# Kernel tuning notes

Measured on AMD Instinct MI355X. Metric: run time of the kernel, lower is better.

## Reference

```python
import jax, jax.numpy as jnp
import numpy as np
import math

B, P, C, PS = 128, 196, 3, 16      # batch, num_patchs, channels, patch_size
HID, HEADS, HD, FF = 768, 12, 64, 3072
RATE = PS // 4                      # highpass_rate = 4 -> rate = 4
EPS = 1e-5


def _local_highpass(x):
    # x: (B, P, HID) -> per-patch FFT highpass, matching LocalHighPass+HighPass.
    img = x.reshape(B, P, C, PS, PS)
    f = jnp.fft.fftshift(jnp.fft.fft2(img, norm='ortho'), axes=(-2, -1))
    mid = PS // 2
    f = f.at[..., mid - RATE:mid + RATE, mid - RATE:mid + RATE].set(0.0)
    out = jnp.fft.ifft2(jnp.fft.ifftshift(f, axes=(-2, -1)), norm='ortho').real
    return out.reshape(B, P, HID)


def _layernorm(x, g, b):
    m = x.mean(-1, keepdims=True)
    v = ((x - m) ** 2).mean(-1, keepdims=True)
    return (x - m) * jax.lax.rsqrt(v + EPS) * g + b


def setup_inputs() -> dict:
    key = jax.random.key(0)
    ks = jax.random.split(key, 16)
    s_h = 1.0 / math.sqrt(HID)
    s_f = 1.0 / math.sqrt(FF)
    inp = {
        'x': jax.random.normal(ks[0], (B, P, HID), jnp.float32),
        'q_w': jax.random.uniform(ks[1], (HID, HID), jnp.float32, -s_h, s_h),
        'q_b': jnp.zeros((HID,), jnp.float32),
        'k_w': jax.random.uniform(ks[2], (HID, HID), jnp.float32, -s_h, s_h),
        'k_b': jnp.zeros((HID,), jnp.float32),
        'v_w': jax.random.uniform(ks[3], (HID, HID), jnp.float32, -s_h, s_h),
        'v_b': jnp.zeros((HID,), jnp.float32),
        'w1': jax.random.uniform(ks[4], (FF, HID), jnp.float32, -s_h, s_h),
        'b1': jnp.zeros((FF,), jnp.float32),
        'w2': jax.random.uniform(ks[5], (HID, FF), jnp.float32, -s_f, s_f),
        'b2': jnp.zeros((HID,), jnp.float32),
        'ln0_g': jnp.ones((HID,), jnp.float32), 'ln0_b': jnp.zeros((HID,), jnp.float32),
        'ln1_g': jnp.ones((HID,), jnp.float32), 'ln1_b': jnp.zeros((HID,), jnp.float32),
        'ln2_g': jnp.ones((HID,), jnp.float32), 'ln2_b': jnp.zeros((HID,), jnp.float32),
    }
    return inp


def reference(x, q_w, q_b, k_w, k_b, v_w, v_b, w1, b1, w2, b2,
              ln0_g, ln0_b, ln1_g, ln1_b, ln2_g, ln2_b):
    hp = _local_highpass(x)                              # (B, P, HID)
    h = _layernorm(hp, ln0_g, ln0_b)
    # MSAttention (first_block=False, so no position embedding add)
    q = (h @ q_w.T + q_b).reshape(B, P, HEADS, HD)
    k = (h @ k_w.T + k_b).reshape(B, P, HEADS, HD)
    v = (h @ v_w.T + v_b).reshape(B, P, HEADS, HD)
    scores = jnp.einsum('bqhd,bkhd->bhqk', q, k) / math.sqrt(HD)
    probs = jax.nn.softmax(scores, axis=-1)
    ctx = jnp.einsum('bhqk,bkhd->bqhd', probs, v).reshape(B, P, HID)
    h2 = hp + _layernorm(ctx, ln1_g, ln1_b)
    mlp = jax.nn.relu(h2 @ w1.T + b1) @ w2.T + b2
    return h2 + _layernorm(mlp, ln2_g, ln2_b)
```

## Files before the change

kernel.cpp:

```cpp
#include <hip/hip_runtime.h>

#define NTOK   25088
#define HIDD   768
#define NHEAD  12
#define HDIM   64
#define FFD    3072
#define NPAT   196
#define QKVS   2304

typedef __attribute__((ext_vector_type(8))) short short8;
typedef __attribute__((ext_vector_type(8))) __bf16 bf16x8;
typedef __attribute__((ext_vector_type(4))) float f32x4;
typedef __attribute__((ext_vector_type(4))) float fl4;
typedef __attribute__((ext_vector_type(4))) unsigned short us4;
typedef __attribute__((ext_vector_type(8))) unsigned short us8;

#define AS1 __attribute__((address_space(1)))
#define AS3 __attribute__((address_space(3)))

__device__ __forceinline__ unsigned short f2bf(float f) {
  unsigned int u = __builtin_bit_cast(unsigned int, f);
  u += 0x7FFFu + ((u >> 16) & 1u);
  return (unsigned short)(u >> 16);
}
__device__ __forceinline__ float bf2f(unsigned short h) {
  unsigned int u = ((unsigned int)h) << 16;
  return __builtin_bit_cast(float, u);
}

template <typename A>
__device__ __forceinline__ auto mfma_sel(A a, A b, f32x4 c, int)
    -> decltype(__builtin_amdgcn_mfma_f32_16x16x32_bf16(a, b, c, 0, 0, 0)) {
  return __builtin_amdgcn_mfma_f32_16x16x32_bf16(a, b, c, 0, 0, 0);
}
template <typename A>
__device__ __forceinline__ auto mfma_sel(A a, A b, f32x4 c, long)
    -> decltype(__builtin_amdgcn_mfma_f32_16x16x32_bf16(
           __builtin_bit_cast(bf16x8, a), __builtin_bit_cast(bf16x8, b), c, 0, 0, 0)) {
  return __builtin_amdgcn_mfma_f32_16x16x32_bf16(
      __builtin_bit_cast(bf16x8, a), __builtin_bit_cast(bf16x8, b), c, 0, 0, 0);
}
__device__ __forceinline__ f32x4 MFMA16(short8 a, short8 b, f32x4 c) {
  return mfma_sel(a, b, c, 0);
}

__device__ __forceinline__ void gload16(const void* g, void* l) {
  __builtin_amdgcn_global_load_lds((const AS1 void*)g, (AS3 void*)l, 16, 0, 0);
}

__device__ __forceinline__ int swz_bid(int nwg) {
  int orig = (int)blockIdx.x;
  int xcd = orig & 7;
  int q = nwg >> 3, r = nwg & 7;
  int base = (xcd < r) ? xcd * (q + 1) : r * (q + 1) + (xcd - r) * q;
  return base + (orig >> 3);
}

__global__ __launch_bounds__(256) void build_M(unsigned short* __restrict__ Mb) {
  __shared__ float Cs[16], Ss[16];
  int t = threadIdx.x;
  if (t < 16) {
    float c = 0.f;
    for (int k = -4; k <= 3; ++k) c += cosf(0.39269908169872414f * (float)(k * t));
    Cs[t] = c;
    Ss[t] = -sinf(1.5707963267948966f * (float)t);
  }
  __syncthreads();
  int r = t >> 4, cc = t & 15;
  for (int j = 0; j < 256; ++j) {
    int dr = (r - (j >> 4)) & 15;
    int dc = (cc - (j & 15)) & 15;
    float val = ((t == j) ? 1.f : 0.f) - (Cs[dr] * Cs[dc] - Ss[dr] * Ss[dc]) * 0.00390625f;
    Mb[t * 256 + j] = f2bf(val);
  }
}

__global__ __launch_bounds__(256) void castk(const float* __restrict__ s,
                                             unsigned short* __restrict__ d, long n4) {
  for (long i = (long)blockIdx.x * 256 + threadIdx.x; i < n4; i += (long)gridDim.x * 256) {
    fl4 v = *(const fl4*)(s + i * 4);
    us4 o;
    o[0] = f2bf(v[0]); o[1] = f2bf(v[1]); o[2] = f2bf(v[2]); o[3] = f2bf(v[3]);
    *(us4*)(d + i * 4) = o;
  }
}

__global__ __launch_bounds__(256) void bias_cat(const float* __restrict__ qb,
                                                const float* __restrict__ kb,
                                                const float* __restrict__ vb,
                                                float* __restrict__ d) {
  for (int i = threadIdx.x; i < QKVS; i += 256)
    d[i] = (i < 768) ? qb[i] : (i < 1536) ? kb[i - 768] : vb[i - 1536];
}

template <int OUT_BF16, int BIAS, int RELU>
__global__ __launch_bounds__(256) void gemm_bt(const unsigned short* __restrict__ A,
                                               const unsigned short* __restrict__ Bm,
                                               const float* __restrict__ bias,
                                               void* __restrict__ Cp,
                                               int Mdim, int Ndim, int Kdim) {
  __shared__ __align__(16) unsigned short As[128 * 32];
  __shared__ __align__(16) unsigned short Bs[128 * 32];
  const int nbn = Ndim >> 7;
  const int bid = swz_bid((int)gridDim.x);
  const int bm = bid / nbn, bn = bid % nbn;
  const int t = threadIdx.x;
  const int lane = t & 63;
  const int w = t >> 6;
  const int wr = (w >> 1) * 64, wc = (w & 1) * 64;
  const int lm = lane & 15, lk = (lane >> 4) * 8;

  f32x4 acc[4][4];
#pragma unroll
  for (int i = 0; i < 4; ++i)
#pragma unroll
    for (int j = 0; j < 4; ++j) acc[i][j] = (f32x4){0.f, 0.f, 0.f, 0.f};

  const unsigned short* Ab = A + (size_t)(bm * 128 + (t >> 2)) * Kdim + (t & 3) * 8;
  const unsigned short* Bb = Bm + (size_t)(bn * 128 + (t >> 2)) * Kdim + (t & 3) * 8;
  unsigned short* AsP = As + t * 8;
  unsigned short* BsP = Bs + t * 8;

  for (int k0 = 0; k0 < Kdim; k0 += 32) {
    gload16(Ab + k0, AsP);
    gload16(Ab + (size_t)64 * Kdim + k0, AsP + 2048);
    gload16(Bb + k0, BsP);
    gload16(Bb + (size_t)64 * Kdim + k0, BsP + 2048);
    asm volatile("s_waitcnt vmcnt(0)" ::: "memory");
    __syncthreads();
    short8 af[4], bfr[4];
#pragma unroll
    for (int mi = 0; mi < 4; ++mi) af[mi] = *(const short8*)&As[(wr + mi * 16 + lm) * 32 + lk];
#pragma unroll
    for (int ni = 0; ni < 4; ++ni) bfr[ni] = *(const short8*)&Bs[(wc + ni * 16 + lm) * 32 + lk];
#pragma unroll
    for (int mi = 0; mi < 4; ++mi)
#pragma unroll
      for (int ni = 0; ni < 4; ++ni) acc[mi][ni] = MFMA16(af[mi], bfr[ni], acc[mi][ni]);
    __syncthreads();
  }

  const int row0 = bm * 128 + wr + (lane >> 4) * 4;
  const int col0 = bn * 128 + wc + lm;
#pragma unroll
  for (int mi = 0; mi < 4; ++mi) {
#pragma unroll
    for (int ni = 0; ni < 4; ++ni) {
      int col = col0 + ni * 16;
      float bia = BIAS ? bias[col] : 0.f;
#pragma unroll
      for (int rg = 0; rg < 4; ++rg) {
        int row = row0 + mi * 16 + rg;
        float vv = acc[mi][ni][rg] + bia;
        if (RELU) vv = vv > 0.f ? vv : 0.f;
        if (OUT_BF16)
          ((unsigned short*)Cp)[(size_t)row * Ndim + col] = f2bf(vv);
        else
          ((float*)Cp)[(size_t)row * Ndim + col] = vv;
      }
    }
  }
}

__global__ __launch_bounds__(256) void ln0_k(const unsigned short* __restrict__ x,
                                             const float* __restrict__ g,
                                             const float* __restrict__ bb,
                                             unsigned short* __restrict__ out) {
  int w = threadIdx.x >> 6, lane = threadIdx.x & 63;
  long row = (long)blockIdx.x * 4 + w;
  const unsigned short* xr = x + row * HIDD;
  float xv[12];
  float s1 = 0.f, s2 = 0.f;
#pragma unroll
  for (int c = 0; c < 3; ++c) {
    us4 u = *(const us4*)(xr + c * 256 + lane * 4);
#pragma unroll
    for (int j = 0; j < 4; ++j) {
      float f = bf2f(u[j]);
      xv[c * 4 + j] = f; s1 += f; s2 += f * f;
    }
  }
#pragma unroll
  for (int off = 32; off; off >>= 1) { s1 += __shfl_xor(s1, off); s2 += __shfl_xor(s2, off); }
  float m = s1 * (1.f / 768.f);
  float rs = rsqrtf(s2 * (1.f / 768.f) - m * m + 1e-5f);
#pragma unroll
  for (int c = 0; c < 3; ++c) {
    int cb = c * 256 + lane * 4;
    us4 o;
#pragma unroll
    for (int j = 0; j < 4; ++j) o[j] = f2bf((xv[c * 4 + j] - m) * rs * g[cb + j] + bb[cb + j]);
    *(us4*)(out + row * HIDD + cb) = o;
  }
}

__global__ __launch_bounds__(256) void ln1_k(const unsigned short* __restrict__ ctx,
                                             const unsigned short* __restrict__ hp,
                                             const float* __restrict__ g,
                                             const float* __restrict__ bb,
                                             float* __restrict__ h2f,
                                             unsigned short* __restrict__ h2b) {
  int w = threadIdx.x >> 6, lane = threadIdx.x & 63;
  long row = (long)blockIdx.x * 4 + w;
  const unsigned short* xr = ctx + row * HIDD;
  float xv[12];
  float s1 = 0.f, s2 = 0.f;
#pragma unroll
  for (int c = 0; c < 3; ++c) {
    us4 u = *(const us4*)(xr + c * 256 + lane * 4);
#pragma unroll
    for (int j = 0; j < 4; ++j) {
      float f = bf2f(u[j]);
      xv[c * 4 + j] = f; s1 += f; s2 += f * f;
    }
  }
#pragma unroll
  for (int off = 32; off; off >>= 1) { s1 += __shfl_xor(s1, off); s2 += __shfl_xor(s2, off); }
  float m = s1 * (1.f / 768.f);
  float rs = rsqrtf(s2 * (1.f / 768.f) - m * m + 1e-5f);
#pragma unroll
  for (int c = 0; c < 3; ++c) {
    int cb = c * 256 + lane * 4;
    us4 hv = *(const us4*)(hp + row * HIDD + cb);
    fl4 o;
    us4 ob;
#pragma unroll
    for (int j = 0; j < 4; ++j) {
      float y = bf2f(hv[j]) + (xv[c * 4 + j] - m) * rs * g[cb + j] + bb[cb + j];
      o[j] = y; ob[j] = f2bf(y);
    }
    *(fl4*)(h2f + row * HIDD + cb) = o;
    *(us4*)(h2b + row * HIDD + cb) = ob;
  }
}

__global__ __launch_bounds__(256) void ln2_k(float* __restrict__ mlp2_out,
                                             const float* __restrict__ h2f,
                                             const float* __restrict__ g,
                                             const float* __restrict__ bb) {
  int w = threadIdx.x >> 6, lane = threadIdx.x & 63;
  long row = (long)blockIdx.x * 4 + w;
  float* xr = mlp2_out + row * HIDD;
  fl4 v[3];
  float s1 = 0.f, s2 = 0.f;
#pragma unroll
  for (int c = 0; c < 3; ++c) {
    v[c] = *(const fl4*)(xr + c * 256 + lane * 4);
#pragma unroll
    for (int j = 0; j < 4; ++j) { s1 += v[c][j]; s2 += v[c][j] * v[c][j]; }
  }
#pragma unroll
  for (int off = 32; off; off >>= 1) { s1 += __shfl_xor(s1, off); s2 += __shfl_xor(s2, off); }
  float m = s1 * (1.f / 768.f);
  float rs = rsqrtf(s2 * (1.f / 768.f) - m * m + 1e-5f);
#pragma unroll
  for (int c = 0; c < 3; ++c) {
    int cb = c * 256 + lane * 4;
    fl4 hv = *(const fl4*)(h2f + row * HIDD + cb);
    fl4 o;
#pragma unroll
    for (int j = 0; j < 4; ++j) o[j] = hv[j] + (v[c][j] - m) * rs * g[cb + j] + bb[cb + j];
    *(fl4*)(xr + cb) = o;
  }
}

__global__ __launch_bounds__(256, 2) void attn_k(const unsigned short* __restrict__ qkv,
                                                 unsigned short* __restrict__ ctx) {
  __shared__ __align__(16) unsigned short Ks[NPAT * 64];
  __shared__ __align__(16) unsigned short VT[64 * 232];
  __shared__ __align__(16) unsigned short PL[4][16 * 40];
  const int b = blockIdx.x / NHEAD, h = blockIdx.x % NHEAD;
  const int t = threadIdx.x, lane = t & 63, w = t >> 6;
  const size_t base = ((size_t)b * NPAT) * QKVS + h * HDIM;

  for (int idx = t; idx < NPAT * 8; idx += 256) {
    int row = idx >> 3, s = idx & 7;
    us8 kv = *(const us8*)&qkv[base + 768 + (size_t)row * QKVS + s * 8];
    *(us8*)((char*)Ks + row * 128 + ((s ^ (row & 7)) << 4)) = kv;
  }
  for (int idx = t; idx < 98 * 64; idx += 256) {
    int pp = idx >> 6, d = idx & 63;
    unsigned int val = (unsigned int)qkv[base + 1536 + (size_t)(2 * pp) * QKVS + d]
                     | ((unsigned int)qkv[base + 1536 + (size_t)(2 * pp + 1) * QKVS + d] << 16);
    *(unsigned int*)&VT[d * 232 + 2 * pp] = val;
  }
  for (int idx = t; idx < 64 * 18; idx += 256) {
    int d = idx / 18, c = idx % 18;
    *(unsigned int*)&VT[d * 232 + 196 + 2 * c] = 0;
  }
  __syncthreads();

  unsigned short* plw = (unsigned short*)PL[w];
  const int lm = lane & 15, lg = lane >> 4, lk = lg * 8;

  for (int qt = w; qt < 13; qt += 4) {
    const int q0 = qt * 16;
    int qrow = q0 + lm; if (qrow > NPAT - 1) qrow = NPAT - 1;
    short8 af0 = *(const short8*)&qkv[base + (size_t)qrow * QKVS + lk];
    short8 af1 = *(const short8*)&qkv[base + (size_t)qrow * QKVS + 32 + lk];

    f32x4 sc[13];
#pragma unroll
    for (int kt = 0; kt < 13; ++kt) {
      int krow = kt * 16 + lm; if (krow > NPAT - 1) krow = NPAT - 1;
      const char* krp = (const char*)Ks + krow * 128;
      short8 b0 = *(const short8*)(krp + (((lg ^ (krow & 7)) & 7) << 4));
      short8 b1 = *(const short8*)(krp + ((((lg + 4) ^ (krow & 7)) & 7) << 4));
      f32x4 z = (f32x4){0.f, 0.f, 0.f, 0.f};
      z = MFMA16(af0, b0, z);
      sc[kt] = MFMA16(af1, b1, z);
    }
#pragma unroll
    for (int kt = 0; kt < 13; ++kt) {
      int col = kt * 16 + lm;
#pragma unroll
      for (int rg = 0; rg < 4; ++rg) {
        float s = sc[kt][rg] * 0.125f;
        sc[kt][rg] = (col < NPAT) ? s : -1e30f;
      }
    }
    float inv[4];
#pragma unroll
    for (int rg = 0; rg < 4; ++rg) {
      float m = -1e30f;
#pragma unroll
      for (int kt = 0; kt < 13; ++kt) m = fmaxf(m, sc[kt][rg]);
      m = fmaxf(m, __shfl_xor(m, 1)); m = fmaxf(m, __shfl_xor(m, 2));
      m = fmaxf(m, __shfl_xor(m, 4)); m = fmaxf(m, __shfl_xor(m, 8));
      float s = 0.f;
#pragma unroll
      for (int kt = 0; kt < 13; ++kt) { float e = __expf(sc[kt][rg] - m); sc[kt][rg] = e; s += e; }
      s += __shfl_xor(s, 1); s += __shfl_xor(s, 2); s += __shfl_xor(s, 4); s += __shfl_xor(s, 8);
      inv[rg] = 1.f / s;
    }

    f32x4 oacc[4];
#pragma unroll
    for (int ni = 0; ni < 4; ++ni) oacc[ni] = (f32x4){0.f, 0.f, 0.f, 0.f};
#pragma unroll
    for (int kc = 0; kc < 7; ++kc) {
#pragma unroll
      for (int sub = 0; sub < 2; ++sub) {
        const int kt = 2 * kc + sub;
#pragma unroll
        for (int rg = 0; rg < 4; ++rg) {
          unsigned short pv_ = 0;
          if (kt < 13) pv_ = f2bf(sc[kt][rg] * inv[rg]);
          plw[(lg * 4 + rg) * 40 + sub * 16 + lm] = pv_;
        }
      }
      asm volatile("s_waitcnt lgkmcnt(0)" ::: "memory");
      __builtin_amdgcn_sched_barrier(0);
      short8 pa = *(const short8*)&plw[lm * 40 + lk];
#pragma unroll
      for (int ni = 0; ni < 4; ++ni) {
        short8 bv = *(const short8*)&VT[(ni * 16 + lm) * 232 + kc * 32 + lk];
        oacc[ni] = MFMA16(pa, bv, oacc[ni]);
      }
    }
#pragma unroll
    for (int rg = 0; rg < 4; ++rg) {
      int r = q0 + lg * 4 + rg;
      if (r < NPAT) {
#pragma unroll
        for (int ni = 0; ni < 4; ++ni)
          ctx[((size_t)b * NPAT + r) * HIDD + h * HDIM + ni * 16 + lm] = f2bf(oacc[ni][rg]);
      }
    }
  }
}

extern "C" void kernel_launch(void* const* d_in, const int* in_sizes, int n_in,
                              void* d_out, int out_size, void* d_ws, size_t ws_size,
                              hipStream_t stream) {
  const float* x    = (const float*)d_in[0];
  const float* q_w  = (const float*)d_in[1];
  const float* q_b  = (const float*)d_in[2];
  const float* k_w  = (const float*)d_in[3];
  const float* k_b  = (const float*)d_in[4];
  const float* v_w  = (const float*)d_in[5];
  const float* v_b  = (const float*)d_in[6];
  const float* w1   = (const float*)d_in[7];
  const float* b1   = (const float*)d_in[8];
  const float* w2   = (const float*)d_in[9];
  const float* b2   = (const float*)d_in[10];
  const float* ln0g = (const float*)d_in[11];
  const float* ln0b = (const float*)d_in[12];
  const float* ln1g = (const float*)d_in[13];
  const float* ln1b = (const float*)d_in[14];
  const float* ln2g = (const float*)d_in[15];
  const float* ln2b = (const float*)d_in[16];

  char* ws = (char*)d_ws;
  size_t o = 0;
  auto alloc = [&](size_t bytes) { size_t r = o; o += (bytes + 255) & ~(size_t)255; return r; };

  const size_t RSZ = (size_t)NTOK * HIDD * 2;
  unsigned short* Mb    = (unsigned short*)(ws + alloc(256 * 256 * 2));
  unsigned short* wqkvb = (unsigned short*)(ws + alloc((size_t)QKVS * HIDD * 2));
  unsigned short* w1b   = (unsigned short*)(ws + alloc((size_t)FFD * HIDD * 2));
  unsigned short* w2b   = (unsigned short*)(ws + alloc((size_t)HIDD * FFD * 2));
  float*          qkvbias = (float*)(ws + alloc(QKVS * 4));
  char* r0 = ws + alloc(RSZ);
  char* r1 = ws + alloc(RSZ);
  char* r2 = ws + alloc(RSZ);
  char* r3 = ws + alloc(RSZ);
  char* r4 = ws + alloc(RSZ);
  char* r5 = ws + alloc(RSZ);
  (void)r5; (void)n_in; (void)in_sizes; (void)ws_size;

  unsigned short* xb  = (unsigned short*)r0;
  unsigned short* hpb = (unsigned short*)r1;
  unsigned short* hb  = (unsigned short*)r2;
  unsigned short* qkv = (unsigned short*)r3;
  unsigned short* cxb = (unsigned short*)r0;
  float*          h2f = (float*)r4;
  unsigned short* h2b = (unsigned short*)r2;
  unsigned short* m1b = (unsigned short*)r0;
  float*          m2f = (float*)d_out;

  build_M<<<1, 256, 0, stream>>>(Mb);
  bias_cat<<<1, 256, 0, stream>>>(q_b, k_b, v_b, qkvbias);

  auto cgrid = [](long n4) { long g = (n4 + 255) / 256; return (int)(g > 2048 ? 2048 : g); };
  long nx4 = (long)NTOK * HIDD / 4;
  castk<<<cgrid(nx4), 256, 0, stream>>>(x, xb, nx4);
  long nw4 = (long)HIDD * HIDD / 4;
  castk<<<cgrid(nw4), 256, 0, stream>>>(q_w, wqkvb, nw4);
  castk<<<cgrid(nw4), 256, 0, stream>>>(k_w, wqkvb + (size_t)768 * HIDD, nw4);
  castk<<<cgrid(nw4), 256, 0, stream>>>(v_w, wqkvb + (size_t)1536 * HIDD, nw4);
  long nf4 = (long)FFD * HIDD / 4;
  castk<<<cgrid(nf4), 256, 0, stream>>>(w1, w1b, nf4);
  castk<<<cgrid(nf4), 256, 0, stream>>>(w2, w2b, nf4);

  gemm_bt<1, 0, 0><<<588 * 2, 256, 0, stream>>>(xb, Mb, nullptr, hpb, 75264, 256, 256);
  ln0_k<<<NTOK / 4, 256, 0, stream>>>(hpb, ln0g, ln0b, hb);

  gemm_bt<1, 1, 0><<<196 * 18, 256, 0, stream>>>(hb, wqkvb, qkvbias, qkv, NTOK, QKVS, HIDD);

  attn_k<<<128 * NHEAD, 256, 0, stream>>>(qkv, cxb);

  ln1_k<<<NTOK / 4, 256, 0, stream>>>(cxb, hpb, ln1g, ln1b, h2f, h2b);

  for (int ch = 0; ch < 2; ++ch) {
    const unsigned short* h2c = h2b + (size_t)ch * 12544 * HIDD;
    float* m2c = m2f + (size_t)ch * 12544 * HIDD;
    gemm_bt<1, 1, 1><<<98 * 24, 256, 0, stream>>>(h2c, w1b, b1, m1b, 12544, FFD, HIDD);
    gemm_bt<0, 1, 0><<<98 * 6, 256, 0, stream>>>(m1b, w2b, b2, m2c, 12544, HIDD, FFD);
  }

  ln2_k<<<NTOK / 4, 256, 0, stream>>>(m2f, h2f, ln2g, ln2b);
  (void)out_size;
}
```

Baseline: 717.0 us.

## Add 256x256-tile double-buffered MFMA GEMM and use it for QKV and MLP

Adds a new bf16 GEMM kernel with 256x256 output tiles, 512 threads, 64-wide K steps and double-buffered 128KB LDS. It uses an XOR-swizzled layout and async global-to-LDS loads, and raises wave priority around the MFMA bursts. The QKV projection and both MLP GEMMs now use it instead of the 128x128 kernel, which should raise arithmetic intensity and cut LDS and global traffic per FLOP. The trade-off is fewer, larger blocks: the FFN2 launch has only 147 blocks per chunk, below the CU count, and the large LDS footprint limits occupancy to one block per CU.

```diff
diff --git a/kernel.cpp b/kernel.cpp
--- a/kernel.cpp
+++ b/kernel.cpp
@@ -144,6 +144,114 @@
   const int col0 = bn * 128 + wc + lm;
 #pragma unroll
   for (int mi = 0; mi < 4; ++mi) {
+#pragma unroll
+    for (int ni = 0; ni < 4; ++ni) {
+      int col = col0 + ni * 16;
+      float bia = BIAS ? bias[col] : 0.f;
+#pragma unroll
+      for (int rg = 0; rg < 4; ++rg) {
+        int row = row0 + mi * 16 + rg;
+        float vv = acc[mi][ni][rg] + bia;
+        if (RELU) vv = vv > 0.f ? vv : 0.f;
+        if (OUT_BF16)
+          ((unsigned short*)Cp)[(size_t)row * Ndim + col] = f2bf(vv);
+        else
+          ((float*)Cp)[(size_t)row * Ndim + col] = vv;
+      }
+    }
+  }
+}
+
+template <int OUT_BF16, int BIAS, int RELU>
+__global__ __launch_bounds__(512, 2) void gemm256(const unsigned short* __restrict__ A,
+                                                  const unsigned short* __restrict__ Bm,
+                                                  const float* __restrict__ bias,
+                                                  void* __restrict__ Cp,
+                                                  int Mdim, int Ndim, int Kdim) {
+  __shared__ __align__(16) char lds[131072];
+  const int nbn = Ndim >> 8;
+  const int bid = swz_bid((int)gridDim.x);
+  const int bm = bid / nbn, bn = bid % nbn;
+  const int t = threadIdx.x;
+  const int lane = t & 63, w = t >> 6;
+  const int wm = w >> 2, wn = w & 3;
+  const int lm = lane & 15, lg = lane >> 4;
+  const int NT = Kdim >> 6;
+
+  const int tr = t >> 3;
+  const int scol = ((t & 7) ^ (tr & 7)) * 8;
+  const unsigned short* Aq = A + (size_t)(bm * 256 + tr) * Kdim + scol;
+  const unsigned short* Bq = Bm + (size_t)(bn * 256 + tr) * Kdim + scol;
+
+  auto STAGE = [&](int kt, int bs) {
+    char* db = lds + bs * 65536;
+#pragma unroll
+    for (int li = 0; li < 4; ++li) {
+      gload16(Aq + (size_t)(li * 64) * Kdim + kt * 64, db + li * 8192 + t * 16);
+      gload16(Bq + (size_t)(li * 64) * Kdim + kt * 64, db + 32768 + li * 8192 + t * 16);
+    }
+  };
+
+  const int sx = lm & 7;
+  int slotb[2];
+#pragma unroll
+  for (int kk = 0; kk < 2; ++kk) slotb[kk] = (((kk << 2) | lg) ^ sx) << 4;
+  const int arow0 = (wm * 128 + lm) * 128;
+  const int brow0 = 32768 + (wn * 64 + lm) * 128;
+
+  f32x4 acc[8][4];
+#pragma unroll
+  for (int i = 0; i < 8; ++i)
+#pragma unroll
+    for (int j = 0; j < 4; ++j) acc[i][j] = (f32x4){0.f, 0.f, 0.f, 0.f};
+
+  STAGE(0, 0);
+  STAGE(1, 1);
+  asm volatile("s_waitcnt vmcnt(8)" ::: "memory");
+  __syncthreads();
+
+  for (int kt = 0; kt < NT; ++kt) {
+    char* db = lds + (kt & 1) * 65536;
+    short8 bq[4][2];
+#pragma unroll
+    for (int ni = 0; ni < 4; ++ni)
+#pragma unroll
+      for (int kk = 0; kk < 2; ++kk)
+        bq[ni][kk] = *(const short8*)(db + brow0 + ni * 2048 + slotb[kk]);
+#pragma unroll
+    for (int q = 0; q < 4; ++q) {
+      short8 aq[2][2];
+#pragma unroll
+      for (int m2 = 0; m2 < 2; ++m2)
+#pragma unroll
+        for (int kk = 0; kk < 2; ++kk)
+          aq[m2][kk] = *(const short8*)(db + arow0 + (q * 2 + m2) * 2048 + slotb[kk]);
+      __builtin_amdgcn_s_setprio(1);
+#pragma unroll
+      for (int m2 = 0; m2 < 2; ++m2)
+#pragma unroll
+        for (int ni = 0; ni < 4; ++ni)
+#pragma unroll
+          for (int kk = 0; kk < 2; ++kk)
+            acc[q * 2 + m2][ni] = MFMA16(aq[m2][kk], bq[ni][kk], acc[q * 2 + m2][ni]);
+      __builtin_amdgcn_s_setprio(0);
+      __builtin_amdgcn_sched_barrier(0);
+    }
+    __syncthreads();
+    if (kt + 2 < NT) {
+      STAGE(kt + 2, kt & 1);
+      asm volatile("s_waitcnt vmcnt(8)" ::: "memory");
+      __syncthreads();
+    } else if (kt + 1 < NT) {
+      asm volatile("s_waitcnt vmcnt(0)" ::: "memory");
+      __syncthreads();
+    }
+  }
+
+  const int row0 = bm * 256 + wm * 128 + lg * 4;
+  const int col0 = bn * 256 + wn * 64 + lm;
+#pragma unroll
+  for (int mi = 0; mi < 8; ++mi) {
 #pragma unroll
     for (int ni = 0; ni < 4; ++ni) {
       int col = col0 + ni * 16;
@@ -436,7 +544,7 @@
   gemm_bt<1, 0, 0><<<588 * 2, 256, 0, stream>>>(xb, Mb, nullptr, hpb, 75264, 256, 256);
   ln0_k<<<NTOK / 4, 256, 0, stream>>>(hpb, ln0g, ln0b, hb);
 
-  gemm_bt<1, 1, 0><<<196 * 18, 256, 0, stream>>>(hb, wqkvb, qkvbias, qkv, NTOK, QKVS, HIDD);
+  gemm256<1, 1, 0><<<98 * 9, 512, 0, stream>>>(hb, wqkvb, qkvbias, qkv, NTOK, QKVS, HIDD);
 
   attn_k<<<128 * NHEAD, 256, 0, stream>>>(qkv, cxb);
 
@@ -445,8 +553,8 @@
   for (int ch = 0; ch < 2; ++ch) {
     const unsigned short* h2c = h2b + (size_t)ch * 12544 * HIDD;
     float* m2c = m2f + (size_t)ch * 12544 * HIDD;
-    gemm_bt<1, 1, 1><<<98 * 24, 256, 0, stream>>>(h2c, w1b, b1, m1b, 12544, FFD, HIDD);
-    gemm_bt<0, 1, 0><<<98 * 6, 256, 0, stream>>>(m1b, w2b, b2, m2c, 12544, HIDD, FFD);
+    gemm256<1, 1, 1><<<49 * 12, 512, 0, stream>>>(h2c, w1b, b1, m1b, 12544, FFD, HIDD);
+    gemm256<0, 1, 0><<<49 * 3, 512, 0, stream>>>(m1b, w2b, b2, m2c, 12544, HIDD, FFD);
   }
 
   ln2_k<<<NTOK / 4, 256, 0, stream>>>(m2f, h2f, ln2g, ln2b);
```

Result: slower. 753.1 us (+5.0%).

## Replace 128x128 GEMM with double-buffered 256x256 tile, swizzled LDS, 8 waves

Applied to the files above, without the earlier changes.

Replaces the simple 128x128x32 single-buffer GEMM with a 256x256 tile kernel using 512 threads, a K-step of 64, XOR-swizzled LDS layout, and double-buffered direct-to-LDS loads interleaved with MFMA quarters. Wait counts, barriers, sched_barrier and setprio are placed so that global loads for the next tiles overlap compute. This removes the fully serialized load-wait-compute loop and the LDS bank conflicts, and raises arithmetic intensity per byte loaded. The trade-off is larger tiles, which give fewer blocks (for example 147 for the FFN2 chunks) and risk poor CU fill, plus 128KB of LDS per block.

```diff
diff --git a/kernel.cpp b/kernel.cpp
--- a/kernel.cpp
+++ b/kernel.cpp
@@ -94,56 +94,112 @@
 }
 
 template <int OUT_BF16, int BIAS, int RELU>
-__global__ __launch_bounds__(256) void gemm_bt(const unsigned short* __restrict__ A,
-                                               const unsigned short* __restrict__ Bm,
-                                               const float* __restrict__ bias,
-                                               void* __restrict__ Cp,
-                                               int Mdim, int Ndim, int Kdim) {
-  __shared__ __align__(16) unsigned short As[128 * 32];
-  __shared__ __align__(16) unsigned short Bs[128 * 32];
-  const int nbn = Ndim >> 7;
+__global__ __launch_bounds__(512, 2) void gemm256(const unsigned short* __restrict__ A,
+                                                  const unsigned short* __restrict__ Bm,
+                                                  const float* __restrict__ bias,
+                                                  void* __restrict__ Cp,
+                                                  int Mdim, int Ndim, int Kdim) {
+  __shared__ __align__(16) char lds[131072];
+  const int nbn = Ndim >> 8;
   const int bid = swz_bid((int)gridDim.x);
   const int bm = bid / nbn, bn = bid % nbn;
   const int t = threadIdx.x;
-  const int lane = t & 63;
-  const int w = t >> 6;
-  const int wr = (w >> 1) * 64, wc = (w & 1) * 64;
-  const int lm = lane & 15, lk = (lane >> 4) * 8;
-
-  f32x4 acc[4][4];
-#pragma unroll
-  for (int i = 0; i < 4; ++i)
+  const int lane = t & 63, w = t >> 6;
+  const int wm = w >> 2, wn = w & 3;
+  const int lm = lane & 15, lg = lane >> 4;
+  const int NT = Kdim >> 6, NITER = NT >> 1;
+
+  const int tr = t >> 3;
+  const int scol = ((t & 7) ^ (tr & 7)) * 8;
+  const unsigned short* Asrc = A + (size_t)(bm * 256 + tr) * Kdim + scol;
+  const unsigned short* Bsrc = Bm + (size_t)(bn * 256 + tr) * Kdim + scol;
+  const size_t K64 = (size_t)64 * Kdim, K128 = (size_t)128 * Kdim, K192 = (size_t)192 * Kdim;
+
+  auto SA = [&](int kt, int d) {
+    char* dst = lds + d * 65536;
+    const unsigned short* s = Asrc + kt * 64;
+    gload16(s, dst + t * 16);
+    gload16(s + K64, dst + 8192 + t * 16);
+    gload16(s + K128, dst + 16384 + t * 16);
+    gload16(s + K192, dst + 24576 + t * 16);
+  };
+  auto SB = [&](int kt, int d, int h) {
+    char* dst = lds + d * 65536 + 32768 + h * 16384;
+    const unsigned short* s = Bsrc + kt * 64 + (h ? K128 : 0);
+    gload16(s, dst + t * 16);
+    gload16(s + K64, dst + 8192 + t * 16);
+  };
+
+  const int sx = lm & 7;
+  int slotb[2];
+#pragma unroll
+  for (int kk = 0; kk < 2; ++kk) slotb[kk] = (((kk << 2) | lg) ^ sx) << 4;
+  const int aoff = wm * 16384 + lm * 128;
+  const int boff = 32768 + (wn >> 1) * 16384 + ((wn & 1) * 64 + lm) * 128;
+
+  f32x4 acc[8][4];
+#pragma unroll
+  for (int i = 0; i < 8; ++i)
 #pragma unroll
     for (int j = 0; j < 4; ++j) acc[i][j] = (f32x4){0.f, 0.f, 0.f, 0.f};
-
-  const unsigned short* Ab = A + (size_t)(bm * 128 + (t >> 2)) * Kdim + (t & 3) * 8;
-  const unsigned short* Bb = Bm + (size_t)(bn * 128 + (t >> 2)) * Kdim + (t & 3) * 8;
-  unsigned short* AsP = As + t * 8;
-  unsigned short* BsP = Bs + t * 8;
-
-  for (int k0 = 0; k0 < Kdim; k0 += 32) {
-    gload16(Ab + k0, AsP);
-    gload16(Ab + (size_t)64 * Kdim + k0, AsP + 2048);
-    gload16(Bb + k0, BsP);
-    gload16(Bb + (size_t)64 * Kdim + k0, BsP + 2048);
-    asm volatile("s_waitcnt vmcnt(0)" ::: "memory");
-    __syncthreads();
-    short8 af[4], bfr[4];
-#pragma unroll
-    for (int mi = 0; mi < 4; ++mi) af[mi] = *(const short8*)&As[(wr + mi * 16 + lm) * 32 + lk];
-#pragma unroll
-    for (int ni = 0; ni < 4; ++ni) bfr[ni] = *(const short8*)&Bs[(wc + ni * 16 + lm) * 32 + lk];
-#pragma unroll
-    for (int mi = 0; mi < 4; ++mi)
-#pragma unroll
-      for (int ni = 0; ni < 4; ++ni) acc[mi][ni] = MFMA16(af[mi], bfr[ni], acc[mi][ni]);
-    __syncthreads();
-  }
-
-  const int row0 = bm * 128 + wr + (lane >> 4) * 4;
-  const int col0 = bn * 128 + wc + lm;
-#pragma unroll
-  for (int mi = 0; mi < 4; ++mi) {
+  short8 bq[4][2];
+
+  auto RDB = [&](const char* db) {
+#pragma unroll
+    for (int ni = 0; ni < 4; ++ni)
+#pragma unroll
+      for (int kk = 0; kk < 2; ++kk)
+        bq[ni][kk] = *(const short8*)(db + boff + ni * 2048 + slotb[kk]);
+  };
+  auto MFMAQ = [&](const char* db, int q, int vmc) {
+    short8 aq[2][2];
+#pragma unroll
+    for (int m2 = 0; m2 < 2; ++m2)
+#pragma unroll
+      for (int kk = 0; kk < 2; ++kk)
+        aq[m2][kk] = *(const short8*)(db + aoff + q * 4096 + m2 * 2048 + slotb[kk]);
+    __builtin_amdgcn_s_barrier();
+    asm volatile("s_waitcnt lgkmcnt(0)" ::: "memory");
+    __builtin_amdgcn_sched_barrier(0);
+    __builtin_amdgcn_s_setprio(1);
+#pragma unroll
+    for (int kk = 0; kk < 2; ++kk)
+#pragma unroll
+      for (int m2 = 0; m2 < 2; ++m2)
+#pragma unroll
+        for (int ni = 0; ni < 4; ++ni)
+          acc[q * 2 + m2][ni] = MFMA16(aq[m2][kk], bq[ni][kk], acc[q * 2 + m2][ni]);
+    __builtin_amdgcn_s_setprio(0);
+    if (vmc == 4) asm volatile("s_waitcnt vmcnt(4)" ::: "memory");
+    else if (vmc == 0) asm volatile("s_waitcnt vmcnt(0)" ::: "memory");
+    __builtin_amdgcn_s_barrier();
+    __builtin_amdgcn_sched_barrier(0);
+  };
+
+  SA(0, 0); SB(0, 0, 0); SB(0, 0, 1); SB(1, 1, 0); SB(1, 1, 1);
+  asm volatile("s_waitcnt vmcnt(4)" ::: "memory");
+  __builtin_amdgcn_s_barrier();
+  __builtin_amdgcn_sched_barrier(0);
+
+  char* d0 = lds;
+  char* d1 = lds + 65536;
+  for (int j = 0; j < NITER; ++j) {
+    const bool nl = (j + 1 < NITER);
+    const int t2 = 2 * j + 2, t3 = 2 * j + 3;
+    RDB(d0); SA(2 * j + 1, 1);   MFMAQ(d0, 0, -1);
+    if (nl) SB(t2, 0, 0);        MFMAQ(d0, 1, -1);
+    if (nl) SB(t2, 0, 1);        MFMAQ(d0, 2, -1);
+                                 MFMAQ(d0, 3, nl ? 4 : 0);
+    RDB(d1); if (nl) SA(t2, 0);  MFMAQ(d1, 0, -1);
+    if (nl) SB(t3, 1, 0);        MFMAQ(d1, 1, -1);
+    if (nl) SB(t3, 1, 1);        MFMAQ(d1, 2, -1);
+                                 MFMAQ(d1, 3, nl ? 4 : -1);
+  }
+
+  const int row0 = bm * 256 + wm * 128 + lg * 4;
+  const int col0 = bn * 256 + wn * 64 + lm;
+#pragma unroll
+  for (int mi = 0; mi < 8; ++mi) {
 #pragma unroll
     for (int ni = 0; ni < 4; ++ni) {
       int col = col0 + ni * 16;
@@ -433,10 +489,10 @@
   castk<<<cgrid(nf4), 256, 0, stream>>>(w1, w1b, nf4);
   castk<<<cgrid(nf4), 256, 0, stream>>>(w2, w2b, nf4);
 
-  gemm_bt<1, 0, 0><<<588 * 2, 256, 0, stream>>>(xb, Mb, nullptr, hpb, 75264, 256, 256);
+  gemm256<1, 0, 0><<<294, 512, 0, stream>>>(xb, Mb, nullptr, hpb, 75264, 256, 256);
   ln0_k<<<NTOK / 4, 256, 0, stream>>>(hpb, ln0g, ln0b, hb);
 
-  gemm_bt<1, 1, 0><<<196 * 18, 256, 0, stream>>>(hb, wqkvb, qkvbias, qkv, NTOK, QKVS, HIDD);
+  gemm256<1, 1, 0><<<98 * 9, 512, 0, stream>>>(hb, wqkvb, qkvbias, qkv, NTOK, QKVS, HIDD);
 
   attn_k<<<128 * NHEAD, 256, 0, stream>>>(qkv, cxb);
 
@@ -445,8 +501,8 @@
   for (int ch = 0; ch < 2; ++ch) {
     const unsigned short* h2c = h2b + (size_t)ch * 12544 * HIDD;
     float* m2c = m2f + (size_t)ch * 12544 * HIDD;
-    gemm_bt<1, 1, 1><<<98 * 24, 256, 0, stream>>>(h2c, w1b, b1, m1b, 12544, FFD, HIDD);
-    gemm_bt<0, 1, 0><<<98 * 6, 256, 0, stream>>>(m1b, w2b, b2, m2c, 12544, HIDD, FFD);
+    gemm256<1, 1, 1><<<49 * 12, 512, 0, stream>>>(h2c, w1b, b1, m1b, 12544, FFD, HIDD);
+    gemm256<0, 1, 0><<<49 * 3, 512, 0, stream>>>(m1b, w2b, b2, m2c, 12544, HIDD, FFD);
   }
 
   ln2_k<<<NTOK / 4, 256, 0, stream>>>(m2f, h2f, ln2g, ln2b);
```

Result: faster. 645.3 us (-10.0%).
